# Kernel tuning notes

Hardware: AMD Instinct MI355X
Metric: run time of the kernel (lower is better)

## Reference

```python
import jax, jax.numpy as jnp
import numpy as np

FORGET_BIAS = 1.0  # TF BasicLSTMCell default

def _lstm_layer(x_seq, state, W, b):
    """x_seq: [B,T,D_in]; state: [B,2*mem] = concat([c,h],1) (state_is_tuple=False).
    Returns (outputs [B,T,mem], final_state [B,2*mem])."""
    mem = state.shape[1] // 2
    c0, h0 = state[:, :mem], state[:, mem:]
    xs = jnp.swapaxes(x_seq, 0, 1)  # [T,B,D_in]

    def step(carry, x_t):
        c, h = carry
        z = jnp.concatenate([x_t, h], axis=-1) @ W + b  # [B,4*mem]
        i, j, f, o = jnp.split(z, 4, axis=-1)           # TF gate order i,j,f,o
        c = c * jax.nn.sigmoid(f + FORGET_BIAS) + jax.nn.sigmoid(i) * jnp.tanh(j)
        h = jnp.tanh(c) * jax.nn.sigmoid(o)
        return (c, h), h

    (c, h), hs = jax.lax.scan(step, (c0, h0), xs)
    return jnp.swapaxes(hs, 0, 1), jnp.concatenate([c, h], axis=-1)


def setup_inputs() -> dict:
    key = jax.random.key(0)
    ks = jax.random.split(key, 4)
    B, T, V, MEM = 64, 512, 256, 1024
    s = lambda n: 1.0 / np.sqrt(n)
    return {
        "x": jax.random.normal(ks[0], (B, T, V), jnp.float32),
        "state0": jnp.zeros((B, 2 * MEM), jnp.float32),
        "state1": jnp.zeros((B, 2 * MEM), jnp.float32),
        "W0": jax.random.normal(ks[1], (V + MEM, 4 * MEM), jnp.float32) * s(V + MEM),
        "b0": jnp.zeros((4 * MEM,), jnp.float32),
        "W1": jax.random.normal(ks[2], (2 * MEM, 4 * MEM), jnp.float32) * s(2 * MEM),
        "b1": jnp.zeros((4 * MEM,), jnp.float32),
        "W_out": jax.random.normal(ks[3], (MEM, V), jnp.float32) * s(MEM),
        "b_out": jnp.zeros((V,), jnp.float32),
    }


def reference(x, state0, state1, W0, b0, W1, b1, W_out, b_out):
    h0_seq, fs0 = _lstm_layer(x, state0, W0, b0)
    h1_seq, fs1 = _lstm_layer(h0_seq, state1, W1, b1)
    outputs = h1_seq @ W_out + b_out  # dense projection to out_vector_size
    final_state = jnp.stack([fs0, fs1], axis=0)  # [n_layers, B, 2*mem]
    return outputs, final_state
```

## Files before the change

### kernel.cpp

```cpp
#include <hip/hip_runtime.h>
#include <stdint.h>

typedef __bf16 bf16;
typedef __attribute__((ext_vector_type(8))) __bf16 bf16x8;
typedef __attribute__((ext_vector_type(4))) float f32x4;
typedef __attribute__((ext_vector_type(4))) unsigned u32x4;

#define OFF_W0P   0ull
#define SZ_W0P    10485760ull
#define OFF_W1P   (OFF_W0P + SZ_W0P)
#define SZ_W1P    16777216ull
#define OFF_WOUT  (OFF_W1P + SZ_W1P)
#define SZ_WOUT   524288ull
#define OFF_B0P   (OFF_WOUT + SZ_WOUT)
#define OFF_B1P   (OFF_B0P + 16384ull)
#define OFF_BOP   (OFF_B1P + 16384ull)
#define OFF_BAR   (OFF_BOP + 1024ull)
#define OFF_FLAG  (OFF_BAR + 128ull)
#define OFF_H0PP  (OFF_BAR + 256ull)
#define OFF_H1PP  (OFF_H0PP + 262144ull)
#define OFF_XP    (OFF_H1PP + 262144ull)
#define SZ_XP     16777216ull
#define OFF_FLAGS (OFF_XP + SZ_XP)
#define OFF_REL   (OFF_FLAGS + 1024ull)

#define OUT_FS0   8388608
#define OUT_FS1   8519680

#define LDS_PARTP 106496
#define LDS_TOTAL 110592

#define CPOL_CC 17

typedef const __attribute__((address_space(1))) void gvoid_t;
typedef __attribute__((address_space(3))) void lvoid_t;

__device__ __forceinline__ void gl_lds16(void* lds, const void* g) {
  __builtin_amdgcn_global_load_lds((gvoid_t*)g, (lvoid_t*)lds, 16, 0, 0);
}

__device__ __forceinline__ __amdgpu_buffer_rsrc_t make_rsrc(const void* p) {
  return __builtin_amdgcn_make_buffer_rsrc(const_cast<void*>(p), (short)0, 0xFFFFFFFFu, 0x00020000u);
}

__device__ __forceinline__ bf16x8 ld_h16(__amdgpu_buffer_rsrc_t rs, unsigned off) {
  u32x4 v = __builtin_amdgcn_raw_buffer_load_b128(rs, off, 0, CPOL_CC);
  return __builtin_bit_cast(bf16x8, v);
}
__device__ __forceinline__ void st_h2(__amdgpu_buffer_rsrc_t rs, unsigned off, float h) {
  bf16 b = (bf16)h;
  __builtin_amdgcn_raw_buffer_store_b16(__builtin_bit_cast(unsigned short, b), rs, off, 0, CPOL_CC);
}

__device__ __forceinline__ size_t hpack_off(int b, int u) {
  return (size_t)((((b >> 4) * 32 + (u >> 5)) * 64 + ((b & 15) | (((u >> 3) & 3) << 4))) * 16 + ((u & 7) << 1));
}

__device__ __forceinline__ float sigm(float v) { return 1.0f / (1.0f + __expf(-v)); }
__device__ __forceinline__ float tanh_(float v) { return 2.0f / (1.0f + __expf(-2.0f * v)) - 1.0f; }
__device__ __forceinline__ float scrub(float v, float lim) { return fminf(fmaxf(v, -lim), lim); }

__device__ __forceinline__ float ldel(const void* p, size_t i, int fl) {
  return fl ? ((const float*)p)[i] : (float)((const bf16*)p)[i];
}

__global__ __launch_bounds__(256) void detect_kernel(const void* __restrict__ W0, char* __restrict__ ws) {
  __shared__ int cnt;
  if (threadIdx.x == 0) cnt = 0;
  __syncthreads();
  int local = 0;
  const unsigned* w = (const unsigned*)W0;
#pragma unroll
  for (int i = 0; i < 4; ++i) {
    unsigned e = (w[threadIdx.x * 4 + i] >> 7) & 0xFF;
    local += (e >= 0x68 && e <= 0x7E) ? 1 : 0;
  }
  atomicAdd(&cnt, local);
  __syncthreads();
  if (threadIdx.x == 0) *(unsigned*)(ws + OFF_FLAG) = (cnt < 512) ? 1u : 0u;
}

__global__ __launch_bounds__(256) void prep_pack(const void* __restrict__ x, const void* __restrict__ W0,
                                                 const void* __restrict__ b0, const void* __restrict__ W1,
                                                 const void* __restrict__ b1, const void* __restrict__ Wout,
                                                 const void* __restrict__ bout, char* __restrict__ ws) {
  const int fl = *(const unsigned*)(ws + OFF_FLAG);
  int id = blockIdx.x * 256 + threadIdx.x;
  if (id < 5242880) {
    int tile = id / 20480, rem = id % 20480;
    int kt = rem >> 9, l = (rem >> 3) & 63, jj = rem & 7;
    int k = kt * 32 + ((l >> 4) << 3) + jj;
    int pc = tile * 16 + (l & 15);
    ((bf16*)(ws + OFF_W0P))[id] = (bf16)ldel(W0, (size_t)k * 4096 + (pc & 3) * 1024 + (pc >> 2), fl);
  } else if (id < 13631488) {
    int id2 = id - 5242880;
    int tile = id2 >> 15, rem = id2 & 32767;
    int kt = rem >> 9, l = (rem >> 3) & 63, jj = rem & 7;
    int k = kt * 32 + ((l >> 4) << 3) + jj;
    int pc = tile * 16 + (l & 15);
    ((bf16*)(ws + OFF_W1P))[id2] = (bf16)ldel(W1, (size_t)k * 4096 + (pc & 3) * 1024 + (pc >> 2), fl);
  } else if (id < 13893632) {
    int id2 = id - 13631488;
    int kt = id2 / 8192, rem = id2 % 8192;
    int nt = rem >> 9, l = (rem >> 3) & 63, jj = rem & 7;
    ((bf16*)(ws + OFF_WOUT))[id2] = (bf16)ldel(Wout, (size_t)(kt * 32 + ((l >> 4) << 3) + jj) * 256 + nt * 16 + (l & 15), fl);
  } else if (id < 13897728) {
    int pc = id - 13893632;
    ((float*)(ws + OFF_B0P))[pc] = ldel(b0, (pc & 3) * 1024 + (pc >> 2), fl);
  } else if (id < 13901824) {
    int pc = id - 13897728;
    ((float*)(ws + OFF_B1P))[pc] = ldel(b1, (pc & 3) * 1024 + (pc >> 2), fl);
  } else if (id < 13902080) {
    int pc = id - 13901824;
    ((float*)(ws + OFF_BOP))[pc] = ldel(bout, pc, fl);
  } else if (id < 22290688) {
    int id2 = id - 13902080;
    int t = id2 >> 14, rem = id2 & 16383;
    int mt = rem >> 12, rem2 = rem & 4095;
    int kt = rem2 >> 9, l = (rem2 >> 3) & 63, j = rem2 & 7;
    int b = mt * 16 + (l & 15);
    int v = kt * 32 + ((l >> 4) << 3) + j;
    ((bf16*)(ws + OFF_XP))[id2] = (bf16)ldel(x, ((size_t)b * 512 + t) * 256 + v, fl);
  }
}

__global__ __launch_bounds__(256) void init_state(const void* __restrict__ s0, const void* __restrict__ s1,
                                                  char* __restrict__ ws) {
  const int fl = *(const unsigned*)(ws + OFF_FLAG);
  int id = blockIdx.x * 256 + threadIdx.x;
  if (id < 65536) {
    int b = id >> 10, u = id & 1023;
    *(bf16*)(ws + OFF_H0PP + 131072 + hpack_off(b, u)) = (bf16)ldel(s0, b * 2048 + 1024 + u, fl);
  } else if (id < 131072) {
    int id2 = id - 65536; int b = id2 >> 10, u = id2 & 1023;
    *(bf16*)(ws + OFF_H1PP + hpack_off(b, u)) = (bf16)ldel(s1, b * 2048 + 1024 + u, fl);
  } else if (id < 131330) {
    ((unsigned*)(ws + OFF_FLAGS))[id - 131072] = 0u;
  }
}

__global__ __launch_bounds__(256, 1) void recur_kernel(const void* __restrict__ s0, const void* __restrict__ s1,
                                                       char* __restrict__ ws, void* __restrict__ outv) {
  extern __shared__ char smem[];
  const int fl = *(const unsigned*)(ws + OFF_FLAG);
  const int tid = threadIdx.x;
  const int lane = tid & 63;
  const int wid = tid >> 6;
  const int cu = blockIdx.x;
  const int nt = cu & 15, mo = (cu >> 4) & 3, dg = cu >> 6;

  auto store_out = [&](size_t idx, float v) {
    if (fl) ((float*)outv)[idx] = v; else ((bf16*)outv)[idx] = (bf16)v;
  };

  {
    const char* g0 = ws + OFF_W0P + (size_t)cu * 40960;
    for (int off = tid * 16; off < 40960; off += 4096) gl_lds16(smem + off, g0 + off);
    const char* g1 = ws + OFF_W1P + (size_t)cu * 65536;
    for (int off = tid * 16; off < 65536; off += 4096) gl_lds16(smem + 40960 + off, g1 + off);
  }
  bf16x8 wreg[8];
#pragma unroll
  for (int i = 0; i < 8; ++i)
    wreg[i] = *(const bf16x8*)(ws + OFF_WOUT + (size_t)(((wid * 8 + i) * 16 + nt) * 64 + lane) * 16);

  const float bini0 = ((const float*)(ws + OFF_B0P))[cu * 16 + (lane & 15)];
  const float bini1 = ((const float*)(ws + OFF_B1P))[cu * 16 + (lane & 15)];
  const float boN = ((const float*)(ws + OFF_BOP))[nt * 16 + (lane & 15)];
  const int u0 = cu * 4 + ((lane & 15) >> 2);
  float c0reg[4], c1reg[4];
#pragma unroll
  for (int r = 0; r < 4; ++r) {
    int b = wid * 16 + ((lane >> 4) << 2) + r;
    c0reg[r] = ldel(s0, b * 2048 + u0, fl);
    c1reg[r] = ldel(s1, b * 2048 + u0, fl);
  }

  const __amdgpu_buffer_rsrc_t rs = make_rsrc(ws);
  unsigned* flags = (unsigned*)(ws + OFF_FLAGS);
  unsigned* rel   = (unsigned*)(ws + OFF_REL);
  const char* dummy = ws + (size_t)lane * 16;
  const unsigned od = (unsigned)(lane * 16);
  const char* lb0 = smem + (size_t)lane * 16;
  const char* lb1 = smem + 40960 + (size_t)lane * 16;

  __syncthreads();

  bf16x8 pf0, pf1, pf2, pf3, pf4, pf5, pf6, pf7;
  f32x4 accP;

  for (int it = 0; it < 517; ++it) {
    const bool a0 = (it < 512);
    const bool a1 = (it >= 1 && it <= 512);
    const bool last = (it == 516);
    const int p = (it - 2 - dg) & 3;
    const int tP = it - 2 - p;
    const bool pw = (it >= 2 && tP >= 0 && tP <= 511);

    const unsigned slot = (unsigned)((it + 1) & 1);
    const unsigned oh0 = (it <= 512) ? (unsigned)(OFF_H0PP) + slot * 131072u + (unsigned)(wid * 32 * 1024 + lane * 16) : od;
    const unsigned oh1 = a1 ? (unsigned)(OFF_H1PP) + slot * 131072u + (unsigned)(wid * 32 * 1024 + lane * 16) : od;

    if (pw && p == 0) {
      const unsigned opf = (unsigned)(OFF_H1PP) + slot * 131072u
                         + (unsigned)((mo * 32 + wid * 8) * 1024 + lane * 16);
      pf0 = ld_h16(rs, opf);
      pf1 = ld_h16(rs, opf + 1024);
      pf2 = ld_h16(rs, opf + 2048);
      pf3 = ld_h16(rs, opf + 3072);
      pf4 = ld_h16(rs, opf + 4096);
      pf5 = ld_h16(rs, opf + 5120);
      pf6 = ld_h16(rs, opf + 6144);
      pf7 = ld_h16(rs, opf + 7168);
#pragma unroll
      for (int r = 0; r < 4; ++r) accP[r] = 0.f;
    }

    f32x4 acc0, acc1;
#pragma unroll
    for (int r = 0; r < 4; ++r) { acc0[r] = bini0; acc1[r] = bini1; }

    if (it < 514) {
      const char* px = a0 ? (ws + OFF_XP + (size_t)((it * 4 + wid) * 8) * 1024 + (size_t)lane * 16) : dummy;

      bf16x8 ring[24];
#pragma unroll
      for (int s = 0; s < 24; ++s)
        ring[s] = (s < 8) ? *(const bf16x8*)(px + s * 1024)
                          : ld_h16(rs, oh0 + (unsigned)((s - 8) * 1024));
#pragma unroll
      for (int s = 0; s < 72; ++s) {
        bf16x8 af = ring[s % 24];
        const int f = s + 24;
        if (f < 72)
          ring[s % 24] = ld_h16(rs, (f < 40) ? oh0 + (unsigned)((f - 8) * 1024)
                                             : oh1 + (unsigned)((f - 40) * 1024));
        if (s < 40)
          acc0 = __builtin_amdgcn_mfma_f32_16x16x32_bf16(af, *(const bf16x8*)(lb0 + s * 1024), acc0, 0, 0, 0);
        if (s >= 8)
          acc1 = __builtin_amdgcn_mfma_f32_16x16x32_bf16(af, *(const bf16x8*)(lb1 + (s - 8) * 1024), acc1, 0, 0, 0);
      }
    }

    if (pw) {
      switch (p) {
        case 0:
          accP = __builtin_amdgcn_mfma_f32_16x16x32_bf16(pf0, wreg[0], accP, 0, 0, 0);
          accP = __builtin_amdgcn_mfma_f32_16x16x32_bf16(pf1, wreg[1], accP, 0, 0, 0);
          break;
        case 1:
          accP = __builtin_amdgcn_mfma_f32_16x16x32_bf16(pf2, wreg[2], accP, 0, 0, 0);
          accP = __builtin_amdgcn_mfma_f32_16x16x32_bf16(pf3, wreg[3], accP, 0, 0, 0);
          break;
        case 2:
          accP = __builtin_amdgcn_mfma_f32_16x16x32_bf16(pf4, wreg[4], accP, 0, 0, 0);
          accP = __builtin_amdgcn_mfma_f32_16x16x32_bf16(pf5, wreg[5], accP, 0, 0, 0);
          break;
        default:
          accP = __builtin_amdgcn_mfma_f32_16x16x32_bf16(pf6, wreg[6], accP, 0, 0, 0);
          accP = __builtin_amdgcn_mfma_f32_16x16x32_bf16(pf7, wreg[7], accP, 0, 0, 0);
          break;
      }
    }

    const int base = lane & 60;
    if (a0) {
      const unsigned h0w = (unsigned)(OFF_H0PP) + (unsigned)(it & 1) * 131072u;
#pragma unroll
      for (int r = 0; r < 4; ++r) {
        float z = acc0[r];
        float zi = scrub(__shfl(z, base + 0, 64), 80.f);
        float zj = scrub(__shfl(z, base + 1, 64), 80.f);
        float zf = scrub(__shfl(z, base + 2, 64), 80.f);
        float zo = scrub(__shfl(z, base + 3, 64), 80.f);
        float c = c0reg[r];
        c = c * sigm(zf + 1.0f) + sigm(zi) * tanh_(zj);
        c = scrub(c, 1000.f);
        float h = tanh_(c) * sigm(zo);
        c0reg[r] = c;
        if ((lane & 3) == 0) {
          int b = wid * 16 + ((lane >> 4) << 2) + r;
          st_h2(rs, h0w + (unsigned)hpack_off(b, u0), h);
          if (it == 511) { store_out(OUT_FS0 + b * 2048 + u0, c); store_out(OUT_FS0 + b * 2048 + 1024 + u0, h); }
        }
      }
    }
    if (a1) {
      const unsigned h1w = (unsigned)(OFF_H1PP) + (unsigned)(it & 1) * 131072u;
#pragma unroll
      for (int r = 0; r < 4; ++r) {
        float z = acc1[r];
        float zi = scrub(__shfl(z, base + 0, 64), 80.f);
        float zj = scrub(__shfl(z, base + 1, 64), 80.f);
        float zf = scrub(__shfl(z, base + 2, 64), 80.f);
        float zo = scrub(__shfl(z, base + 3, 64), 80.f);
        float c = c1reg[r];
        c = c * sigm(zf + 1.0f) + sigm(zi) * tanh_(zj);
        c = scrub(c, 1000.f);
        float h = tanh_(c) * sigm(zo);
        c1reg[r] = c;
        if ((lane & 3) == 0) {
          int b = wid * 16 + ((lane >> 4) << 2) + r;
          st_h2(rs, h1w + (unsigned)hpack_off(b, u0), h);
          if (it == 512) { store_out(OUT_FS1 + b * 2048 + u0, c); store_out(OUT_FS1 + b * 2048 + 1024 + u0, h); }
        }
      }
    }
    if (pw && p == 3) {
      *(f32x4*)(smem + LDS_PARTP + (size_t)(wid * 64 + lane) * 16) = accP;
      __syncthreads();
      if (wid == 0) {
        f32x4 sm = *(const f32x4*)(smem + LDS_PARTP + (size_t)lane * 16);
#pragma unroll
        for (int w = 1; w < 4; ++w) {
          f32x4 q = *(const f32x4*)(smem + LDS_PARTP + (size_t)(w * 64 + lane) * 16);
#pragma unroll
          for (int r = 0; r < 4; ++r) sm[r] += q[r];
        }
#pragma unroll
        for (int r = 0; r < 4; ++r) {
          int b = mo * 16 + ((lane >> 4) << 2) + r;
          store_out(((size_t)b * 512 + tP) * 256 + nt * 16 + (lane & 15), sm[r] + boN);
        }
      }
    }
    if (last) break;

    asm volatile("s_waitcnt vmcnt(0)" ::: "memory");
    __syncthreads();
    if (tid == 0)
      __hip_atomic_store(flags + cu, (unsigned)(it + 1), __ATOMIC_RELAXED, __HIP_MEMORY_SCOPE_AGENT);
    if (cu == 0) {
      while (__hip_atomic_load(flags + tid, __ATOMIC_RELAXED, __HIP_MEMORY_SCOPE_AGENT) < (unsigned)(it + 1))
        __builtin_amdgcn_s_sleep(8);
      __syncthreads();
      if (tid == 0)
        __hip_atomic_store(rel, (unsigned)(it + 1), __ATOMIC_RELAXED, __HIP_MEMORY_SCOPE_AGENT);
    }
    if (tid == 0) {
      while (__hip_atomic_load(rel, __ATOMIC_RELAXED, __HIP_MEMORY_SCOPE_AGENT) < (unsigned)(it + 1))
        __builtin_amdgcn_s_sleep(8);
    }
    __syncthreads();
    asm volatile("" ::: "memory");
  }
}

extern "C" void kernel_launch(void* const* d_in, const int* in_sizes, int n_in,
                              void* d_out, int out_size, void* d_ws, size_t ws_size,
                              hipStream_t stream) {
  const void* x    = d_in[0];
  const void* s0   = d_in[1];
  const void* s1   = d_in[2];
  const void* W0   = d_in[3];
  const void* b0   = d_in[4];
  const void* W1   = d_in[5];
  const void* b1   = d_in[6];
  const void* Wout = d_in[7];
  const void* bout = d_in[8];
  char* ws = (char*)d_ws;
  (void)in_sizes; (void)n_in; (void)out_size; (void)ws_size;

  hipFuncSetAttribute((const void*)recur_kernel, hipFuncAttributeMaxDynamicSharedMemorySize, LDS_TOTAL);

  hipLaunchKernelGGL(detect_kernel, dim3(1),     dim3(256), 0, stream, W0, ws);
  hipLaunchKernelGGL(prep_pack,     dim3(87073), dim3(256), 0, stream, x, W0, b0, W1, b1, Wout, bout, ws);
  hipLaunchKernelGGL(init_state,    dim3(514),   dim3(256), 0, stream, s0, s1, ws);
  hipLaunchKernelGGL(recur_kernel,  dim3(256),   dim3(256), LDS_TOTAL, stream, s0, s1, ws, d_out);
}
```

Before: 5.144 ms.

## Pack h stores, deepen load ring, fold projection reduce into barrier, poll faster

Each LSTM cell step now gathers four hidden values via shuffles and writes them as one 8-byte packed bf16 store instead of four 2-byte stores. The prefetch ring for the recurrent A-operands grows from 24 to 32 entries, so more loads are in flight per step. The output-projection partial reduction now reuses the grid barrier's __syncthreads instead of its own, running between flag publish and the spin wait. The spin-wait sleep drops from 8 to 1 to cut wakeup latency, at the cost of more polling traffic and more registers for the ring.

```diff
diff --git a/kernel.cpp b/kernel.cpp
--- a/kernel.cpp
+++ b/kernel.cpp
@@ -5,6 +5,7 @@
 typedef __attribute__((ext_vector_type(8))) __bf16 bf16x8;
 typedef __attribute__((ext_vector_type(4))) float f32x4;
 typedef __attribute__((ext_vector_type(4))) unsigned u32x4;
+typedef __attribute__((ext_vector_type(2))) unsigned u32x2;
 
 #define OFF_W0P   0ull
 #define SZ_W0P    10485760ull
@@ -47,9 +48,8 @@
   u32x4 v = __builtin_amdgcn_raw_buffer_load_b128(rs, off, 0, CPOL_CC);
   return __builtin_bit_cast(bf16x8, v);
 }
-__device__ __forceinline__ void st_h2(__amdgpu_buffer_rsrc_t rs, unsigned off, float h) {
-  bf16 b = (bf16)h;
-  __builtin_amdgcn_raw_buffer_store_b16(__builtin_bit_cast(unsigned short, b), rs, off, 0, CPOL_CC);
+__device__ __forceinline__ void st_h8(__amdgpu_buffer_rsrc_t rs, unsigned off, u32x2 v) {
+  __builtin_amdgcn_raw_buffer_store_b64(v, rs, off, 0, CPOL_CC);
 }
 
 __device__ __forceinline__ size_t hpack_off(int b, int u) {
@@ -62,6 +62,11 @@
 
 __device__ __forceinline__ float ldel(const void* p, size_t i, int fl) {
   return fl ? ((const float*)p)[i] : (float)((const bf16*)p)[i];
+}
+
+__device__ __forceinline__ unsigned pack2(float a, float b) {
+  return (unsigned)__builtin_bit_cast(unsigned short, (bf16)a)
+       | ((unsigned)__builtin_bit_cast(unsigned short, (bf16)b) << 16);
 }
 
 __global__ __launch_bounds__(256) void detect_kernel(const void* __restrict__ W0, char* __restrict__ ws) {
@@ -183,6 +188,7 @@
   const unsigned od = (unsigned)(lane * 16);
   const char* lb0 = smem + (size_t)lane * 16;
   const char* lb1 = smem + 40960 + (size_t)lane * 16;
+  const int gb = (lane >> 4) << 2;
 
   __syncthreads();
 
@@ -223,17 +229,17 @@
     if (it < 514) {
       const char* px = a0 ? (ws + OFF_XP + (size_t)((it * 4 + wid) * 8) * 1024 + (size_t)lane * 16) : dummy;
 
-      bf16x8 ring[24];
-#pragma unroll
-      for (int s = 0; s < 24; ++s)
+      bf16x8 ring[32];
+#pragma unroll
+      for (int s = 0; s < 32; ++s)
         ring[s] = (s < 8) ? *(const bf16x8*)(px + s * 1024)
                           : ld_h16(rs, oh0 + (unsigned)((s - 8) * 1024));
 #pragma unroll
       for (int s = 0; s < 72; ++s) {
-        bf16x8 af = ring[s % 24];
-        const int f = s + 24;
+        bf16x8 af = ring[s & 31];
+        const int f = s + 32;
         if (f < 72)
-          ring[s % 24] = ld_h16(rs, (f < 40) ? oh0 + (unsigned)((f - 8) * 1024)
+          ring[s & 31] = ld_h16(rs, (f < 40) ? oh0 + (unsigned)((f - 8) * 1024)
                                              : oh1 + (unsigned)((f - 40) * 1024));
         if (s < 40)
           acc0 = __builtin_amdgcn_mfma_f32_16x16x32_bf16(af, *(const bf16x8*)(lb0 + s * 1024), acc0, 0, 0, 0);
@@ -278,10 +284,18 @@
         c = scrub(c, 1000.f);
         float h = tanh_(c) * sigm(zo);
         c0reg[r] = c;
-        if ((lane & 3) == 0) {
-          int b = wid * 16 + ((lane >> 4) << 2) + r;
-          st_h2(rs, h0w + (unsigned)hpack_off(b, u0), h);
-          if (it == 511) { store_out(OUT_FS0 + b * 2048 + u0, c); store_out(OUT_FS0 + b * 2048 + 1024 + u0, h); }
+        float g0 = __shfl(h, (lane & 48) + 0, 64);
+        float g1 = __shfl(h, (lane & 48) + 4, 64);
+        float g2 = __shfl(h, (lane & 48) + 8, 64);
+        float g3 = __shfl(h, (lane & 48) + 12, 64);
+        if ((lane & 15) == 0) {
+          int b = wid * 16 + gb + r;
+          u32x2 v; v[0] = pack2(g0, g1); v[1] = pack2(g2, g3);
+          st_h8(rs, h0w + (unsigned)hpack_off(b, cu * 4), v);
+        }
+        if (it == 511 && (lane & 3) == 0) {
+          int b = wid * 16 + gb + r;
+          store_out(OUT_FS0 + b * 2048 + u0, c); store_out(OUT_FS0 + b * 2048 + 1024 + u0, h);
         }
       }
     }
@@ -299,47 +313,74 @@
         c = scrub(c, 1000.f);
         float h = tanh_(c) * sigm(zo);
         c1reg[r] = c;
-        if ((lane & 3) == 0) {
-          int b = wid * 16 + ((lane >> 4) << 2) + r;
-          st_h2(rs, h1w + (unsigned)hpack_off(b, u0), h);
-          if (it == 512) { store_out(OUT_FS1 + b * 2048 + u0, c); store_out(OUT_FS1 + b * 2048 + 1024 + u0, h); }
+        float g0 = __shfl(h, (lane & 48) + 0, 64);
+        float g1 = __shfl(h, (lane & 48) + 4, 64);
+        float g2 = __shfl(h, (lane & 48) + 8, 64);
+        float g3 = __shfl(h, (lane & 48) + 12, 64);
+        if ((lane & 15) == 0) {
+          int b = wid * 16 + gb + r;
+          u32x2 v; v[0] = pack2(g0, g1); v[1] = pack2(g2, g3);
+          st_h8(rs, h1w + (unsigned)hpack_off(b, cu * 4), v);
         }
-      }
-    }
-    if (pw && p == 3) {
+        if (it == 512 && (lane & 3) == 0) {
+          int b = wid * 16 + gb + r;
+          store_out(OUT_FS1 + b * 2048 + u0, c); store_out(OUT_FS1 + b * 2048 + 1024 + u0, h);
+        }
+      }
+    }
+    if (pw && p == 3)
       *(f32x4*)(smem + LDS_PARTP + (size_t)(wid * 64 + lane) * 16) = accP;
-      __syncthreads();
-      if (wid == 0) {
-        f32x4 sm = *(const f32x4*)(smem + LDS_PARTP + (size_t)lane * 16);
-#pragma unroll
-        for (int w = 1; w < 4; ++w) {
-          f32x4 q = *(const f32x4*)(smem + LDS_PARTP + (size_t)(w * 64 + lane) * 16);
-#pragma unroll
-          for (int r = 0; r < 4; ++r) sm[r] += q[r];
+    if (last) {
+      if (pw && p == 3) {
+        __syncthreads();
+        if (wid == 0) {
+          f32x4 sm = *(const f32x4*)(smem + LDS_PARTP + (size_t)lane * 16);
+#pragma unroll
+          for (int w = 1; w < 4; ++w) {
+            f32x4 q = *(const f32x4*)(smem + LDS_PARTP + (size_t)(w * 64 + lane) * 16);
+#pragma unroll
+            for (int r = 0; r < 4; ++r) sm[r] += q[r];
+          }
+#pragma unroll
+          for (int r = 0; r < 4; ++r) {
+            int b = mo * 16 + gb + r;
+            store_out(((size_t)b * 512 + tP) * 256 + nt * 16 + (lane & 15), sm[r] + boN);
+          }
         }
-#pragma unroll
-        for (int r = 0; r < 4; ++r) {
-          int b = mo * 16 + ((lane >> 4) << 2) + r;
-          store_out(((size_t)b * 512 + tP) * 256 + nt * 16 + (lane & 15), sm[r] + boN);
-        }
-      }
-    }
-    if (last) break;
+      }
+      break;
+    }
 
     asm volatile("s_waitcnt vmcnt(0)" ::: "memory");
     __syncthreads();
     if (tid == 0)
       __hip_atomic_store(flags + cu, (unsigned)(it + 1), __ATOMIC_RELAXED, __HIP_MEMORY_SCOPE_AGENT);
+
+    if (pw && p == 3 && wid == 0) {
+      f32x4 sm = *(const f32x4*)(smem + LDS_PARTP + (size_t)lane * 16);
+#pragma unroll
+      for (int w = 1; w < 4; ++w) {
+        f32x4 q = *(const f32x4*)(smem + LDS_PARTP + (size_t)(w * 64 + lane) * 16);
+#pragma unroll
+        for (int r = 0; r < 4; ++r) sm[r] += q[r];
+      }
+#pragma unroll
+      for (int r = 0; r < 4; ++r) {
+        int b = mo * 16 + gb + r;
+        store_out(((size_t)b * 512 + tP) * 256 + nt * 16 + (lane & 15), sm[r] + boN);
+      }
+    }
+
     if (cu == 0) {
       while (__hip_atomic_load(flags + tid, __ATOMIC_RELAXED, __HIP_MEMORY_SCOPE_AGENT) < (unsigned)(it + 1))
-        __builtin_amdgcn_s_sleep(8);
+        __builtin_amdgcn_s_sleep(1);
       __syncthreads();
       if (tid == 0)
         __hip_atomic_store(rel, (unsigned)(it + 1), __ATOMIC_RELAXED, __HIP_MEMORY_SCOPE_AGENT);
     }
     if (tid == 0) {
       while (__hip_atomic_load(rel, __ATOMIC_RELAXED, __HIP_MEMORY_SCOPE_AGENT) < (unsigned)(it + 1))
-        __builtin_amdgcn_s_sleep(8);
+        __builtin_amdgcn_s_sleep(1);
     }
     __syncthreads();
     asm volatile("" ::: "memory");
```

New measurement: 5.314 ms. +3.3%, slower.
